# Kernel tuning notes

Hardware: AMD Instinct MI355X
Metric: run time of the kernel (lower is better)

Reference implementation:

```python
import math
import jax, jax.numpy as jnp
import numpy as np

B, L, D, H, FF = 32, 796, 512, 8, 2048
HD = D // H          # 64
CS, STRIDE = 16, 13  # clip_size=16, overlap_area_size=3 -> stride 13
NC = (L - CS) // STRIDE + 1  # 61 clips, tiles L exactly


def _ln(v):
    m = jnp.mean(v, axis=-1, keepdims=True)
    s = jnp.mean((v - m) ** 2, axis=-1, keepdims=True)
    return (v - m) / jnp.sqrt(s + 1e-6)


def setup_inputs() -> dict:
    key = jax.random.key(0)
    ks = iter(jax.random.split(key, 64))
    def w(*shape):
        return jax.random.normal(next(ks), shape, jnp.float32) * 0.02
    inp = {
        "x": jax.random.normal(next(ks), (B, L, D), jnp.float32),
        "mask": jnp.ones((B, 1, L), dtype=bool),
        # global block params
        "g_ln_g": jnp.ones((D,), jnp.float32), "g_ln_b": jnp.zeros((D,), jnp.float32),
        "Wq": w(D, D), "Wk": w(D, D), "Wv": w(D, D), "Wo": w(D, D),
        "bq": jnp.zeros((D,), jnp.float32), "bk": jnp.zeros((D,), jnp.float32),
        "bv": jnp.zeros((D,), jnp.float32), "bo": jnp.zeros((D,), jnp.float32),
        "f_ln_g": jnp.ones((D,), jnp.float32), "f_ln_b": jnp.zeros((D,), jnp.float32),
        "W1": w(D, FF), "b1": jnp.zeros((FF,), jnp.float32),
        "W2": w(FF, D), "b2": jnp.zeros((D,), jnp.float32),
        # per-batch-element clip params (ModuleList of 32 -> stacked leading dim B)
        "c_ln_g": jnp.ones((B, D), jnp.float32), "c_ln_b": jnp.zeros((B, D), jnp.float32),
        "cWq": w(B, D, D), "cWk": w(B, D, D), "cWv": w(B, D, D), "cWo": w(B, D, D),
        "cbq": jnp.zeros((B, D), jnp.float32), "cbk": jnp.zeros((B, D), jnp.float32),
        "cbv": jnp.zeros((B, D), jnp.float32), "cbo": jnp.zeros((B, D), jnp.float32),
        "cf_ln_g": jnp.ones((B, D), jnp.float32), "cf_ln_b": jnp.zeros((B, D), jnp.float32),
        "cW1": w(B, D, FF), "cb1": jnp.zeros((B, FF), jnp.float32),
        "cW2": w(B, FF, D), "cb2": jnp.zeros((B, D), jnp.float32),
    }
    return inp


def reference(x, mask, g_ln_g, g_ln_b, Wq, Wk, Wv, Wo, bq, bk, bv, bo,
              f_ln_g, f_ln_b, W1, b1, W2, b2,
              c_ln_g, c_ln_b, cWq, cWk, cWv, cWo, cbq, cbk, cbv, cbo,
              cf_ln_g, cf_ln_b, cW1, cb1, cW2, cb2):
    # ---- clip partition: overlapping length-16 windows, stride 13 ----
    starts = np.arange(NC) * STRIDE
    idx = starts[:, None] + np.arange(CS)            # [NC, CS]
    clips = x[:, idx]                                 # [B, NC, CS, D]
    cmask = mask[:, 0][:, idx]                        # [B, NC, CS]
    # channel shuffle on last 384 dims: view(nc,16,24,16).permute(0,3,2,1)
    c1 = clips[..., :128]
    c2 = clips[..., 128:].reshape(B, NC, CS, 24, 16)
    c2 = jnp.transpose(c2, (0, 1, 4, 3, 2)).reshape(B, NC, CS, 384)
    clips = jnp.concatenate([c1, c2], axis=-1)        # [B, NC, CS, D]
    # ---- per-batch-element clip LN + MHA + FFN (distinct weights per b) ----
    cn = _ln(clips) * c_ln_g[:, None, None, :] + c_ln_b[:, None, None, :]
    q = (jnp.einsum('bncd,bde->bnce', cn, cWq) + cbq[:, None, None, :]).reshape(B, NC, CS, H, HD)
    k = (jnp.einsum('bncd,bde->bnce', cn, cWk) + cbk[:, None, None, :]).reshape(B, NC, CS, H, HD)
    v = (jnp.einsum('bncd,bde->bnce', cn, cWv) + cbv[:, None, None, :]).reshape(B, NC, CS, H, HD)
    q = q / math.sqrt(HD)
    sc = jnp.einsum('bnqhd,bnkhd->bnhqk', q, k)       # [B, NC, H, CS, CS]
    sc = jnp.where(cmask[:, :, None, None, :], sc, -jnp.inf)
    a = jax.nn.softmax(sc, axis=-1)
    ctx = jnp.einsum('bnhqk,bnkhd->bnqhd', a, v).reshape(B, NC, CS, D)
    mh = jnp.einsum('bncd,bde->bnce', ctx, cWo) + cbo[:, None, None, :]
    hcl = mh + clips                                  # dropout = identity (eval)
    fn = _ln(hcl) * cf_ln_g[:, None, None, :] + cf_ln_b[:, None, None, :]
    fmid = jax.nn.relu(jnp.einsum('bncd,bdf->bncf', fn, cW1) + cb1[:, None, None, :])
    clips_out = jnp.einsum('bncf,bfd->bncd', fmid, cW2) + cb2[:, None, None, :] + hcl
    p = np.arange(L)
    cidx = np.minimum(p // STRIDE, NC - 1)
    off = p - cidx * STRIDE
    x_rec = clips_out[:, cidx, off]                   # [B, L, D]
    # ---- global LN + MHA + residual + FFN ----
    xn = _ln(x_rec) * g_ln_g + g_ln_b
    q2 = (xn @ Wq + bq).reshape(B, L, H, HD) / math.sqrt(HD)
    k2 = (xn @ Wk + bk).reshape(B, L, H, HD)
    v2 = (xn @ Wv + bv).reshape(B, L, H, HD)
    sc2 = jnp.einsum('bqhd,bkhd->bhqk', q2, k2)
    sc2 = jnp.where(mask[:, None, :, :], sc2, -jnp.inf)
    ctx2 = jnp.einsum('bhqk,bkhd->bqhd', jax.nn.softmax(sc2, axis=-1), v2).reshape(B, L, D)
    h = ctx2 @ Wo + bo + x
    hn = _ln(h) * f_ln_g + f_ln_b
    o = jax.nn.relu(hn @ W1 + b1) @ W2 + b2 + h
    return o
```

## Files before the change

### kernel.cpp

```cpp
#include <hip/hip_runtime.h>

#define B_   32
#define L_   796
#define D_   512
#define H_   8
#define HD_  64
#define FF_  2048
#define CS_  16
#define STR_ 13
#define NC_  61
#define NQT_ 13
#define MC_  976
#define QKVS 1536
#define QS   (0.125f * 1.44269504f)

typedef __attribute__((ext_vector_type(8))) short short8;
typedef __attribute__((ext_vector_type(4))) float f32x4;

__device__ __forceinline__ unsigned short f2bf(float x) {
    unsigned u = __float_as_uint(x);
    unsigned r = u + 0x7FFFu + ((u >> 16) & 1u);
    return (unsigned short)(r >> 16);
}
__device__ __forceinline__ float bf2f(unsigned short h) {
    return __uint_as_float(((unsigned)h) << 16);
}
__device__ __forceinline__ float ex2(float x) {
    return __builtin_amdgcn_exp2f(x);
}
__device__ __forceinline__ void gload16(const unsigned short* g, unsigned short* l) {
    __builtin_amdgcn_global_load_lds(
        (const __attribute__((address_space(1))) void*)g,
        (__attribute__((address_space(3))) void*)l, 16, 0, 0);
}

__global__ __launch_bounds__(256) void k_ln(const float* __restrict__ in,
                                            unsigned short* __restrict__ out,
                                            const float* __restrict__ gamma,
                                            const float* __restrict__ beta,
                                            int rows_per_batch, int gstride, int gather)
{
    __shared__ float red[8];
    long long row = blockIdx.x;
    int tid = threadIdx.x;
    int b;
    float v0, v1;
    if (gather == 2) {
        b = (int)(row / MC_);
        int rr = (int)(row % MC_);
        int n = rr >> 4, c = rr & 15;
        long long xb = (long long)b * L_ * D_;
        int d0 = tid, st0, sd0;
        if (d0 < 128) { st0 = n * STR_ + c; sd0 = d0; }
        else { int j = d0 - 128; st0 = n * STR_ + (j & 15); sd0 = 128 + ((j >> 4) << 4) + c; }
        v0 = in[xb + (long long)st0 * D_ + sd0];
        int j1 = tid + 128;
        int st1 = n * STR_ + (j1 & 15), sd1 = 128 + ((j1 >> 4) << 4) + c;
        v1 = in[xb + (long long)st1 * D_ + sd1];
    } else {
        long long srow = row;
        if (gather == 1) {
            int p = (int)(row % L_);
            b = (int)(row / L_);
            int ci = p / STR_; if (ci > NC_ - 1) ci = NC_ - 1;
            srow = ((long long)b * NC_ + ci) * CS_ + (p - ci * STR_);
        } else {
            b = (int)(row / rows_per_batch);
        }
        const float* xr = in + srow * D_;
        v0 = xr[tid]; v1 = xr[tid + 256];
    }
    float s = v0 + v1;
#pragma unroll
    for (int off = 1; off < 64; off <<= 1) s += __shfl_xor(s, off);
    if ((tid & 63) == 0) red[tid >> 6] = s;
    __syncthreads();
    float mean = (red[0] + red[1] + red[2] + red[3]) * (1.0f / 512.0f);
    float d0 = v0 - mean, d1 = v1 - mean;
    float vv = d0 * d0 + d1 * d1;
#pragma unroll
    for (int off = 1; off < 64; off <<= 1) vv += __shfl_xor(vv, off);
    if ((tid & 63) == 0) red[4 + (tid >> 6)] = vv;
    __syncthreads();
    float var = (red[4] + red[5] + red[6] + red[7]) * (1.0f / 512.0f);
    float rstd = rsqrtf(var + 1e-6f);
    const float* g  = gamma + (long long)b * gstride;
    const float* bt = beta  + (long long)b * gstride;
    unsigned short* o = out + row * D_;
    o[tid]       = f2bf(d0 * rstd * g[tid]       + bt[tid]);
    o[tid + 256] = f2bf(d1 * rstd * g[tid + 256] + bt[tid + 256]);
}

__global__ __launch_bounds__(256) void k_wt(const float* __restrict__ W,
                                            unsigned short* __restrict__ T,
                                            int rowStride, int tStride,
                                            long long sWb, long long sTb)
{
    __shared__ float t[32][33];
    int z = blockIdx.z;
    const float* Wz = W + (long long)z * sWb;
    unsigned short* Tz = T + (long long)z * sTb;
    int n0 = blockIdx.x << 5, k0 = blockIdx.y << 5;
    int tx = threadIdx.x & 31, ty = threadIdx.x >> 5;
#pragma unroll
    for (int i = 0; i < 4; i++) {
        int k = ty + (i << 3);
        t[k][tx] = Wz[(long long)(k0 + k) * rowStride + n0 + tx];
    }
    __syncthreads();
#pragma unroll
    for (int i = 0; i < 4; i++) {
        int n = ty + (i << 3);
        Tz[(long long)(n0 + n) * tStride + k0 + tx] = f2bf(t[tx][n]);
    }
}

__global__ __launch_bounds__(256) void k_wt_stack(const float* __restrict__ Wa,
                                                  const float* __restrict__ Wb,
                                                  const float* __restrict__ Wc,
                                                  const float* __restrict__ Wd,
                                                  unsigned short* __restrict__ T,
                                                  int nb, int ntens, long long sWb)
{
    __shared__ float t[32][33];
    int z = blockIdx.z;
    int tt = z / nb, b = z % nb;
    const float* Wz = (tt == 0 ? Wa : tt == 1 ? Wb : tt == 2 ? Wc : Wd)
                      + (long long)b * sWb;
    unsigned short* Tz = T + ((long long)b * ntens + tt) * (512 * 512);
    int n0 = blockIdx.x << 5, k0 = blockIdx.y << 5;
    int tx = threadIdx.x & 31, ty = threadIdx.x >> 5;
#pragma unroll
    for (int i = 0; i < 4; i++) {
        int k = ty + (i << 3);
        t[k][tx] = Wz[(long long)(k0 + k) * 512 + n0 + tx];
    }
    __syncthreads();
#pragma unroll
    for (int i = 0; i < 4; i++) {
        int n = ty + (i << 3);
        Tz[(long long)(n0 + n) * 512 + k0 + tx] = f2bf(t[tx][n]);
    }
}

__global__ __launch_bounds__(512) void k_gemm_mfma(
    const unsigned short* __restrict__ A, const unsigned short* __restrict__ WT,
    const float* __restrict__ b0p, const float* __restrict__ b1p,
    const float* __restrict__ b2p,
    const float* res, const float* __restrict__ xg, void* Cout,
    int M, int N, int K, int ldwk, int NX, int NYd, int mode,
    long long sAb, long long sWb, long long sBb, long long sRb, long long sCb,
    float alpha, float alpha1, int relu, int biasmode, int resmode, int outbf16)
{
    __shared__ unsigned short lds[16384];
    int tid = threadIdx.x;

    int bid = blockIdx.x;
    int xcd = bid & 7, inner = bid >> 3;
    int x = inner % NX, t = inner / NX;
    int y, z;
    if (mode == 0) { y = t % NYd; z = (t / NYd) * 8 + xcd; }
    else           { y = t * 8 + xcd; z = 0; }
    int row0 = y << 7, col0 = x << 7;
    if (row0 >= M) return;

    const unsigned short* Ab = A + z * sAb;
    const unsigned short* Wb = WT + z * sWb;

    int w = tid >> 6, lane = tid & 63;
    int wr = (w >> 2) << 6;
    int wc = (w & 3) << 5;
    int l15 = lane & 15, lg = lane >> 4;
    int lrow4 = lane >> 2, lslot = lane & 3;

    f32x4 acc[4][2];
#pragma unroll
    for (int i = 0; i < 4; i++)
#pragma unroll
        for (int j = 0; j < 2; j++) acc[i][j] = (f32x4)0.f;

    const int nt = K >> 5;
    int srow = (w << 4) + lrow4;
    int skey = (srow >> 1) & 3;

#pragma unroll
    for (int pt = 0; pt < 2; ++pt) {
        int k0 = pt << 5;
        unsigned short* sA = lds + (pt << 13);
        unsigned short* sW = sA + 4096;
        gload16(Ab + (long long)(row0 + srow) * K + k0 + ((lslot ^ skey) << 3),
                sA + ((w << 4) << 5));
        gload16(Wb + (long long)(col0 + srow) * ldwk + k0 + ((lslot ^ skey) << 3),
                sW + ((w << 4) << 5));
    }

    for (int kt = 0; kt < nt; ++kt) {
        if (kt + 1 < nt) asm volatile("s_waitcnt vmcnt(2)" ::: "memory");
        else             asm volatile("s_waitcnt vmcnt(0)" ::: "memory");
        __builtin_amdgcn_s_barrier();

        unsigned short* lA = lds + ((kt & 1) << 13);
        unsigned short* lW = lA + 4096;

        short8 af[4], bfr[2];
#pragma unroll
        for (int mf = 0; mf < 4; mf++) {
            int r = wr + (mf << 4) + l15;
            af[mf] = *(const short8*)(lA + (r << 5) + ((lg ^ ((r >> 1) & 3)) << 3));
        }
#pragma unroll
        for (int nf = 0; nf < 2; nf++) {
            int r = wc + (nf << 4) + l15;
            bfr[nf] = *(const short8*)(lW + (r << 5) + ((lg ^ ((r >> 1) & 3)) << 3));
        }

        asm volatile("s_waitcnt lgkmcnt(0)" ::: "memory");
        __builtin_amdgcn_s_barrier();

        if (kt + 2 < nt) {
            int k0 = (kt + 2) << 5;
            gload16(Ab + (long long)(row0 + srow) * K + k0 + ((lslot ^ skey) << 3),
                    lA + ((w << 4) << 5));
            gload16(Wb + (long long)(col0 + srow) * ldwk + k0 + ((lslot ^ skey) << 3),
                    lW + ((w << 4) << 5));
        }

        __builtin_amdgcn_s_setprio(1);
#pragma unroll
        for (int mf = 0; mf < 4; mf++)
#pragma unroll
            for (int nf = 0; nf < 2; nf++)
                acc[mf][nf] = __builtin_amdgcn_mfma_f32_16x16x32_bf16(
                    af[mf], bfr[nf], acc[mf][nf], 0, 0, 0);
        __builtin_amdgcn_s_setprio(0);
    }

#pragma unroll
    for (int mf = 0; mf < 4; mf++) {
#pragma unroll
        for (int reg = 0; reg < 4; reg++) {
            int gr = row0 + wr + (mf << 4) + (lg << 2) + reg;
            if (gr >= M) continue;
#pragma unroll
            for (int nf = 0; nf < 2; nf++) {
                int gc = col0 + wc + (nf << 4) + l15;
                float v = acc[mf][nf][reg];
                if (biasmode == 1) v += b0p[z * sBb + gc];
                else if (biasmode == 3) {
                    const float* bp = gc < 512 ? b0p : (gc < 1024 ? b1p : b2p);
                    v += bp[z * sBb + (gc & 511)];
                }
                v *= (gc < 512) ? alpha : alpha1;
                if (relu) v = fmaxf(v, 0.f);
                if (resmode == 1) {
                    v += res[z * sRb + (long long)gr * N + gc];
                } else if (resmode == 2) {
                    int n = gr >> 4, c = gr & 15;
                    int st, sd;
                    if (gc < 128) { st = n * STR_ + c; sd = gc; }
                    else {
                        int jj = gc - 128;
                        st = n * STR_ + (jj & 15);
                        sd = 128 + ((jj >> 4) << 4) + c;
                    }
                    v += xg[((long long)z * L_ + st) * D_ + sd];
                }
                long long co = z * sCb + (long long)gr * N + gc;
                if (outbf16) ((unsigned short*)Cout)[co] = f2bf(v);
                else         ((float*)Cout)[co] = v;
            }
        }
    }
}

__global__ __launch_bounds__(256) void k_clip_attn(const unsigned short* __restrict__ qkv,
                                                   unsigned short* __restrict__ ctx)
{
    __shared__ float qs[CS_][65], ks[CS_][65], vs[CS_][65], ps[CS_][17];
    int id = blockIdx.x;
    int h = id & (H_ - 1);
    int n = (id / H_) % NC_;
    int b = id / (H_ * NC_);
    long long base = (((long long)b * NC_ + n) * CS_) * QKVS + h * HD_;
    int tid = threadIdx.x;
#pragma unroll
    for (int i = 0; i < 4; i++) {
        int e = tid + i * 256;
        int r = e >> 6, c = e & 63;
        long long ro = base + (long long)r * QKVS + c;
        qs[r][c] = bf2f(qkv[ro]);
        ks[r][c] = bf2f(qkv[ro + 512]);
        vs[r][c] = bf2f(qkv[ro + 1024]);
    }
    __syncthreads();
    int qr = tid >> 4, kc = tid & 15;
    float s = 0.f;
#pragma unroll
    for (int d = 0; d < HD_; d++) s += qs[qr][d] * ks[kc][d];
    float m = s;
#pragma unroll
    for (int off = 1; off < 16; off <<= 1) m = fmaxf(m, __shfl_xor(m, off));
    float e = ex2(s - m);
    float sum = e;
#pragma unroll
    for (int off = 1; off < 16; off <<= 1) sum += __shfl_xor(sum, off);
    ps[qr][kc] = e / sum;
    __syncthreads();
    int dg = (tid & 15) * 4;
    float o0 = 0, o1 = 0, o2 = 0, o3 = 0;
#pragma unroll
    for (int kk = 0; kk < CS_; kk++) {
        float pp = ps[qr][kk];
        o0 += pp * vs[kk][dg + 0];
        o1 += pp * vs[kk][dg + 1];
        o2 += pp * vs[kk][dg + 2];
        o3 += pp * vs[kk][dg + 3];
    }
    long long ob = ((((long long)b * NC_ + n) * CS_) + qr) * D_ + h * HD_ + dg;
    ctx[ob + 0] = f2bf(o0);
    ctx[ob + 1] = f2bf(o1);
    ctx[ob + 2] = f2bf(o2);
    ctx[ob + 3] = f2bf(o3);
}

__global__ __launch_bounds__(256) void k_flash_mfma(
    const unsigned short* __restrict__ qkv,
    unsigned short* __restrict__ out)
{
    __shared__ unsigned short lQ[4096], lK[4096], lV[4096], lP[4096];
    int bid = blockIdx.x;
    int h  = bid & 7;
    int inner = bid >> 3;
    int qt = inner % NQT_;
    int b  = inner / NQT_;
    int tid = threadIdx.x;
    int q0 = qt * 64;
    long long base = (long long)b * L_ * QKVS + h * HD_;

    int w = tid >> 6, lane = tid & 63;
    int l15 = lane & 15, lg = lane >> 4;
    int lrow = lane >> 3, lslot = lane & 7;
    int srow = lane;
    int sd0  = w << 4;

#pragma unroll
    for (int i = 0; i < 2; i++) {
        int cb = (w << 4) + (i << 3);
        int rr = cb + lrow;
        gload16(qkv + base + (long long)(q0 + rr) * QKVS + ((lslot ^ (rr & 7)) << 3),
                lQ + (cb << 6));
    }
    __syncthreads();

    int qrow = (w << 4) + l15;
    short8 qf[2];
#pragma unroll
    for (int ks = 0; ks < 2; ks++) {
        int slot = (ks << 2) + lg;
        qf[ks] = *(const short8*)(lQ + qrow * 64 + ((slot ^ (qrow & 7)) << 3));
    }
    unsigned short* lPw = lP + (w << 10);

    float m[4], l[4];
    f32x4 oacc[4];
#pragma unroll
    for (int r = 0; r < 4; r++) { m[r] = -1e30f; l[r] = 0.f; }
#pragma unroll
    for (int nf = 0; nf < 4; nf++) oacc[nf] = (f32x4)0.f;

    for (int kt = 0; kt < NQT_; kt++) {
        int k0 = kt * 64;
        __syncthreads();
#pragma unroll
        for (int i = 0; i < 2; i++) {
            int cb = (w << 4) + (i << 3);
            int rr = cb + lrow;
            gload16(qkv + base + 512 + (long long)(k0 + rr) * QKVS + ((lslot ^ (rr & 7)) << 3),
                    lK + (cb << 6));
        }
        {
            int gr = k0 + srow;
            short8 v0 = (short8)0, v1 = (short8)0;
            if (gr < L_) {
                const unsigned short* pv = qkv + base + 1024 + (long long)gr * QKVS + sd0;
                v0 = *(const short8*)pv;
                v1 = *(const short8*)(pv + 8);
            }
            int ts = srow >> 3, t7 = srow & 7;
#pragma unroll
            for (int i = 0; i < 8; i++) {
                int d = sd0 + i;
                lV[d * 64 + ((ts ^ (d & 7)) << 3) + t7] = (unsigned short)v0[i];
            }
#pragma unroll
            for (int i = 0; i < 8; i++) {
                int d = sd0 + 8 + i;
                lV[d * 64 + ((ts ^ (d & 7)) << 3) + t7] = (unsigned short)v1[i];
            }
        }
        __syncthreads();

        f32x4 acc[4];
#pragma unroll
        for (int nf = 0; nf < 4; nf++) {
            acc[nf] = (f32x4)0.f;
            int tok = (nf << 4) + l15;
            int key = tok & 7;
#pragma unroll
            for (int ks = 0; ks < 2; ks++) {
                int slot = (ks << 2) + lg;
                short8 kf = *(const short8*)(lK + tok * 64 + ((slot ^ key) << 3));
                acc[nf] = __builtin_amdgcn_mfma_f32_16x16x32_bf16(qf[ks], kf, acc[nf], 0, 0, 0);
            }
        }
        float rm[4];
#pragma unroll
        for (int r = 0; r < 4; r++) rm[r] = -1e30f;
#pragma unroll
        for (int nf = 0; nf < 4; nf++) {
            bool oob = (k0 + (nf << 4) + l15) >= L_;
#pragma unroll
            for (int r = 0; r < 4; r++) {
                if (oob) acc[nf][r] = -1e30f;
                rm[r] = fmaxf(rm[r], acc[nf][r]);
            }
        }
#pragma unroll
        for (int off = 1; off < 16; off <<= 1) {
#pragma unroll
            for (int r = 0; r < 4; r++) rm[r] = fmaxf(rm[r], __shfl_xor(rm[r], off));
        }
        float sc[4], ls[4];
#pragma unroll
        for (int r = 0; r < 4; r++) {
            float mn = fmaxf(m[r], rm[r]);
            sc[r] = ex2(m[r] - mn);
            m[r] = mn;
            ls[r] = 0.f;
        }
#pragma unroll
        for (int nf = 0; nf < 4; nf++) {
            int tok = (nf << 4) + l15;
            int slot = tok >> 3, t7 = tok & 7;
#pragma unroll
            for (int r = 0; r < 4; r++) {
                float p = ex2(acc[nf][r] - m[r]);
                ls[r] += p;
                int row = (lg << 2) + r;
                lPw[row * 64 + ((slot ^ (row & 7)) << 3) + t7] = f2bf(p);
            }
        }
#pragma unroll
        for (int off = 1; off < 16; off <<= 1) {
#pragma unroll
            for (int r = 0; r < 4; r++) ls[r] += __shfl_xor(ls[r], off);
        }
#pragma unroll
        for (int r = 0; r < 4; r++) l[r] = l[r] * sc[r] + ls[r];
#pragma unroll
        for (int nf = 0; nf < 4; nf++) {
#pragma unroll
            for (int r = 0; r < 4; r++) oacc[nf][r] *= sc[r];
        }
#pragma unroll
        for (int ks = 0; ks < 2; ks++) {
            int slot = (ks << 2) + lg;
            short8 pa = *(const short8*)(lPw + l15 * 64 + ((slot ^ (l15 & 7)) << 3));
#pragma unroll
            for (int nf = 0; nf < 4; nf++) {
                int d = (nf << 4) + l15;
                short8 vb = *(const short8*)(lV + d * 64 + ((slot ^ (d & 7)) << 3));
                oacc[nf] = __builtin_amdgcn_mfma_f32_16x16x32_bf16(pa, vb, oacc[nf], 0, 0, 0);
            }
        }
    }
    long long obase = (long long)b * L_ * D_ + h * HD_;
#pragma unroll
    for (int r = 0; r < 4; r++) {
        int gr = q0 + (w << 4) + (lg << 2) + r;
        if (gr >= L_) continue;
        float inv = 1.f / l[r];
        long long ob = obase + (long long)gr * D_;
#pragma unroll
        for (int nf = 0; nf < 4; nf++)
            out[ob + (nf << 4) + l15] = f2bf(oacc[nf][r] * inv);
    }
}

static inline void gemm(hipStream_t st, const unsigned short* A, const unsigned short* WTp,
                        const float* b0, const float* b1, const float* b2,
                        const float* res, const float* xg, void* C,
                        int M, int N, int K, int ldwk, int G,
                        long long sAb, long long sWb, long long sBb,
                        long long sRb, long long sCb,
                        float alpha, float alpha1, int relu, int biasmode,
                        int resmode, int outbf16)
{
    int NX = N / 128;
    int NY = (M + 127) >> 7;
    int mode = (G > 1) ? 0 : 1;
    int NYp = mode ? ((NY + 7) & ~7) : NY;
    int nblk = mode ? (NYp * NX) : (G * NY * NX);
    k_gemm_mfma<<<nblk, 512, 0, st>>>(A, WTp, b0, b1, b2, res, xg, C,
                                      M, N, K, ldwk, NX, NY, mode,
                                      sAb, sWb, sBb, sRb, sCb,
                                      alpha, alpha1, relu, biasmode, resmode, outbf16);
}

extern "C" void kernel_launch(void* const* d_in, const int* in_sizes, int n_in,
                              void* d_out, int out_size, void* d_ws, size_t ws_size,
                              hipStream_t stream)
{
    (void)in_sizes; (void)n_in; (void)out_size; (void)ws_size;
    const float* x      = (const float*)d_in[0];
    const float* g_ln_g = (const float*)d_in[2];
    const float* g_ln_b = (const float*)d_in[3];
    const float* Wq = (const float*)d_in[4];
    const float* Wk = (const float*)d_in[5];
    const float* Wv = (const float*)d_in[6];
    const float* Wo = (const float*)d_in[7];
    const float* bq = (const float*)d_in[8];
    const float* bk = (const float*)d_in[9];
    const float* bv = (const float*)d_in[10];
    const float* bo = (const float*)d_in[11];
    const float* f_ln_g = (const float*)d_in[12];
    const float* f_ln_b = (const float*)d_in[13];
    const float* W1 = (const float*)d_in[14];
    const float* b1 = (const float*)d_in[15];
    const float* W2 = (const float*)d_in[16];
    const float* b2 = (const float*)d_in[17];
    const float* c_ln_g = (const float*)d_in[18];
    const float* c_ln_b = (const float*)d_in[19];
    const float* cWq = (const float*)d_in[20];
    const float* cWk = (const float*)d_in[21];
    const float* cWv = (const float*)d_in[22];
    const float* cWo = (const float*)d_in[23];
    const float* cbq = (const float*)d_in[24];
    const float* cbk = (const float*)d_in[25];
    const float* cbv = (const float*)d_in[26];
    const float* cbo = (const float*)d_in[27];
    const float* cf_ln_g = (const float*)d_in[28];
    const float* cf_ln_b = (const float*)d_in[29];
    const float* cW1 = (const float*)d_in[30];
    const float* cb1 = (const float*)d_in[31];
    const float* cW2 = (const float*)d_in[32];
    const float* cb2 = (const float*)d_in[33];

    char* wsb = (char*)d_ws;
    float*          bA   = (float*)wsb;
    unsigned short* bB   = (unsigned short*)(wsb + (64ll  << 20));
    unsigned short* bQKV = (unsigned short*)(wsb + (96ll  << 20));
    unsigned short* wT   = (unsigned short*)(wsb + (188ll << 20));

    const long long sA   = (long long)MC_ * D_;
    const long long sQKV = (long long)MC_ * QKVS;
    const long long sWW  = (long long)D_ * D_;
    const int MG = B_ * L_;

    k_ln<<<B_ * MC_, 256, 0, stream>>>(x, bB, c_ln_g, c_ln_b, MC_, D_, 2);
    k_wt_stack<<<dim3(16, 16, 3 * B_), 256, 0, stream>>>(cWq, cWk, cWv, nullptr,
                                                         wT, B_, 3, sWW);
    gemm(stream, bB, wT, cbq, cbk, cbv, nullptr, nullptr, bQKV,
         MC_, QKVS, D_, D_, B_, sA, 3 * sWW, D_, 0, sQKV,
         QS, 1.0f, 0, 3, 0, 1);
    k_clip_attn<<<B_ * NC_ * H_, 256, 0, stream>>>(bQKV, bB);
    k_wt<<<dim3(16, 16, B_), 256, 0, stream>>>(cWo, wT, D_, D_, sWW, sWW);
    gemm(stream, bB, wT, cbo, nullptr, nullptr, nullptr, x, bA,
         MC_, D_, D_, D_, B_, sA, sWW, D_, 0, sA,
         1.0f, 1.0f, 0, 1, 2, 0);
    k_ln<<<B_ * MC_, 256, 0, stream>>>(bA, bB, cf_ln_g, cf_ln_b, MC_, D_, 0);
    for (int c = 0; c < 2; c++) {
        k_wt<<<dim3(32, 16, B_), 256, 0, stream>>>(cW1 + c * 1024, wT, FF_, D_,
                                                   (long long)D_ * FF_, 1024ll * D_);
        gemm(stream, bB, wT, cb1 + c * 1024, nullptr, nullptr, nullptr, nullptr, bQKV,
             MC_, 1024, D_, D_, B_, sA, 1024ll * D_, FF_, 0, (long long)MC_ * 1024,
             1.0f, 1.0f, 1, 1, 0, 1);
        k_wt<<<dim3(16, 32, B_), 256, 0, stream>>>(cW2 + (long long)c * 1024 * D_, wT,
                                                   D_, 1024, (long long)FF_ * D_,
                                                   (long long)D_ * 1024);
        gemm(stream, bQKV, wT, cb2, nullptr, nullptr, bA, nullptr, bA,
             MC_, D_, 1024, 1024, B_, (long long)MC_ * 1024, (long long)D_ * 1024,
             D_, sA, sA, 1.0f, 1.0f, 0, (c == 0) ? 1 : 0, 1, 0);
    }

    unsigned short* gQKVO = wT;
    unsigned short* gW1   = wT + 4 * 262144;
    unsigned short* gW2   = wT + 8 * 262144;
    k_wt_stack<<<dim3(16, 16, 4), 256, 0, stream>>>(Wq, Wk, Wv, Wo, gQKVO, 1, 4, 0);
    k_wt<<<dim3(64, 16, 1), 256, 0, stream>>>(W1, gW1, FF_, D_, 0, 0);
    k_wt<<<dim3(16, 64, 1), 256, 0, stream>>>(W2, gW2, D_, FF_, 0, 0);

    k_ln<<<MG, 256, 0, stream>>>(bA, bB, g_ln_g, g_ln_b, L_, 0, 1);
    gemm(stream, bB, gQKVO, bq, bk, bv, nullptr, nullptr, bQKV,
         MG, QKVS, D_, D_, 1, 0, 0, 0, 0, 0,
         QS, 1.0f, 0, 3, 0, 1);
    k_flash_mfma<<<B_ * H_ * NQT_, 256, 0, stream>>>(bQKV, bB);
    gemm(stream, bB, gQKVO + 3 * 262144, bo, nullptr, nullptr, x, nullptr, bA,
         MG, D_, D_, D_, 1, 0, 0, 0, 0, 0,
         1.0f, 1.0f, 0, 1, 1, 0);
    k_ln<<<MG, 256, 0, stream>>>(bA, bB, f_ln_g, f_ln_b, MG, 0, 0);
    for (int c = 0; c < 2; c++) {
        gemm(stream, bB, gW1 + (long long)c * 1024 * 512, b1 + c * 1024,
             nullptr, nullptr, nullptr, nullptr, bQKV,
             MG, 1024, D_, D_, 1, 0, 0, 0, 0, 0,
             1.0f, 1.0f, 1, 1, 0, 1);
        gemm(stream, bQKV, gW2 + c * 1024, b2, nullptr, nullptr,
             (c == 0) ? bA : (float*)d_out, nullptr, d_out,
             MG, D_, 1024, FF_, 1, 0, 0, 0, 0, 0,
             1.0f, 1.0f, 0, (c == 0) ? 1 : 0, 1, 0);
    }
}
```

Before: 1.382 ms.

## Lazy softmax rescale in flash attention, reuse Q LDS for P, tighten GEMM bounds

The flash attention kernel now rescales the running max and output accumulators only when some row's new max exceeds the old one by more than a threshold (FA4-style lazy rescaling), checked wave-wide with a ballot. The out-of-bounds key masking runs only on the last key tile. The P buffer reuses the Q LDS region after Q is loaded into registers, cutting LDS per block. The GEMM kernel also gets a min-blocks hint in its launch bounds. Skipping rescales risks larger unnormalized exponent values, which the threshold bounds, and the occupancy hint may force register spills.

```diff
diff --git a/kernel.cpp b/kernel.cpp
--- a/kernel.cpp
+++ b/kernel.cpp
@@ -143,7 +143,7 @@
     }
 }
 
-__global__ __launch_bounds__(512) void k_gemm_mfma(
+__global__ __launch_bounds__(512, 8) void k_gemm_mfma(
     const unsigned short* __restrict__ A, const unsigned short* __restrict__ WT,
     const float* __restrict__ b0p, const float* __restrict__ b1p,
     const float* __restrict__ b2p,
@@ -327,7 +327,10 @@
     const unsigned short* __restrict__ qkv,
     unsigned short* __restrict__ out)
 {
-    __shared__ unsigned short lQ[4096], lK[4096], lV[4096], lP[4096];
+    __shared__ unsigned short sh[12288];
+    unsigned short* lQ = sh;
+    unsigned short* lK = sh + 4096;
+    unsigned short* lV = sh + 8192;
     int bid = blockIdx.x;
     int h  = bid & 7;
     int inner = bid >> 3;
@@ -359,7 +362,8 @@
         int slot = (ks << 2) + lg;
         qf[ks] = *(const short8*)(lQ + qrow * 64 + ((slot ^ (qrow & 7)) << 3));
     }
-    unsigned short* lPw = lP + (w << 10);
+    asm volatile("s_waitcnt lgkmcnt(0)" ::: "memory");
+    unsigned short* lPw = lQ + (w << 10);
 
     float m[4], l[4];
     f32x4 oacc[4];
@@ -413,31 +417,45 @@
                 acc[nf] = __builtin_amdgcn_mfma_f32_16x16x32_bf16(qf[ks], kf, acc[nf], 0, 0, 0);
             }
         }
+        if (kt == NQT_ - 1) {
+#pragma unroll
+            for (int nf = 0; nf < 4; nf++) {
+                bool oob = (k0 + (nf << 4) + l15) >= L_;
+#pragma unroll
+                for (int r = 0; r < 4; r++)
+                    if (oob) acc[nf][r] = -1e30f;
+            }
+        }
         float rm[4];
 #pragma unroll
         for (int r = 0; r < 4; r++) rm[r] = -1e30f;
 #pragma unroll
         for (int nf = 0; nf < 4; nf++) {
-            bool oob = (k0 + (nf << 4) + l15) >= L_;
+#pragma unroll
+            for (int r = 0; r < 4; r++) rm[r] = fmaxf(rm[r], acc[nf][r]);
+        }
+#pragma unroll
+        for (int off = 1; off < 16; off <<= 1) {
+#pragma unroll
+            for (int r = 0; r < 4; r++) rm[r] = fmaxf(rm[r], __shfl_xor(rm[r], off));
+        }
+        bool need = false;
+#pragma unroll
+        for (int r = 0; r < 4; r++) need = need || (rm[r] > m[r] + 8.0f);
+        if (__ballot(need)) {
 #pragma unroll
             for (int r = 0; r < 4; r++) {
-                if (oob) acc[nf][r] = -1e30f;
-                rm[r] = fmaxf(rm[r], acc[nf][r]);
-            }
-        }
-#pragma unroll
-        for (int off = 1; off < 16; off <<= 1) {
-#pragma unroll
-            for (int r = 0; r < 4; r++) rm[r] = fmaxf(rm[r], __shfl_xor(rm[r], off));
-        }
-        float sc[4], ls[4];
-#pragma unroll
-        for (int r = 0; r < 4; r++) {
-            float mn = fmaxf(m[r], rm[r]);
-            sc[r] = ex2(m[r] - mn);
-            m[r] = mn;
-            ls[r] = 0.f;
-        }
+                float mn = fmaxf(m[r], rm[r]);
+                float sc = ex2(m[r] - mn);
+                m[r] = mn;
+                l[r] *= sc;
+#pragma unroll
+                for (int nf = 0; nf < 4; nf++) oacc[nf][r] *= sc;
+            }
+        }
+        float ls[4];
+#pragma unroll
+        for (int r = 0; r < 4; r++) ls[r] = 0.f;
 #pragma unroll
         for (int nf = 0; nf < 4; nf++) {
             int tok = (nf << 4) + l15;
@@ -456,12 +474,7 @@
             for (int r = 0; r < 4; r++) ls[r] += __shfl_xor(ls[r], off);
         }
 #pragma unroll
-        for (int r = 0; r < 4; r++) l[r] = l[r] * sc[r] + ls[r];
-#pragma unroll
-        for (int nf = 0; nf < 4; nf++) {
-#pragma unroll
-            for (int r = 0; r < 4; r++) oacc[nf][r] *= sc[r];
-        }
+        for (int r = 0; r < 4; r++) l[r] += ls[r];
 #pragma unroll
         for (int ks = 0; ks < 2; ks++) {
             int slot = (ks << 2) + lg;
```

New measurement: 1.530 ms. +10.7%, slower.
